# Optimization experiments

Hardware: AMD Instinct MI355X
Metric: run time of the kernel (lower is better)

The kernel has to match this reference:

```python
import jax, jax.numpy as jnp
import numpy as np

D = 1024       # num_feature == heads*dim_head
NHEADS = 16
HD = 64
INNER = NHEADS * HD
FF = 2048      # hardcoded mlp_dim in CSGO_model
L = 4          # depth
NOUT = 26      # hardcoded number of InvDynamic heads
IDH = 512      # inverse_dynamic_dim
B = 64
T = 32         # horizon


def _ln(x, g=None, b=None, eps=1e-5):
    mu = jnp.mean(x, axis=-1, keepdims=True)
    var = jnp.mean((x - mu) ** 2, axis=-1, keepdims=True)
    y = (x - mu) * jax.lax.rsqrt(var + eps)
    if g is not None:
        y = y * g + b
    return y


def setup_inputs() -> dict:
    key = jax.random.key(0)
    ks = jax.random.split(key, 20)
    s = 0.02
    inp = {
        'x': jax.random.normal(ks[0], (B, T, D), jnp.float32),
        # transformer params, stacked over depth L
        'qkv_w': jax.random.normal(ks[1], (L, D, 3 * INNER), jnp.float32) * s,
        'out_w': jax.random.normal(ks[2], (L, INNER, D), jnp.float32) * s,
        'out_b': jnp.zeros((L, D), jnp.float32),
        'attn_ln_g': jnp.ones((L, D), jnp.float32),
        'attn_ln_b': jnp.zeros((L, D), jnp.float32),
        'ff_ln_g': jnp.ones((L, D), jnp.float32),
        'ff_ln_b': jnp.zeros((L, D), jnp.float32),
        'ff_w1': jax.random.normal(ks[3], (L, D, FF), jnp.float32) * s,
        'ff_b1': jnp.zeros((L, FF), jnp.float32),
        'ff_w2': jax.random.normal(ks[4], (L, FF, D), jnp.float32) * s,
        'ff_b2': jnp.zeros((L, D), jnp.float32),
        # 26 InvDynamic heads, stacked
        'head_w1': jax.random.normal(ks[5], (NOUT, 2 * D, IDH), jnp.float32) * s,
        'head_b1': jnp.zeros((NOUT, IDH), jnp.float32),
        'head_w2': jax.random.normal(ks[6], (NOUT, IDH, IDH), jnp.float32) * s,
        'head_b2': jnp.zeros((NOUT, IDH), jnp.float32),
        'head_w3': jax.random.normal(ks[7], (NOUT, IDH, 1), jnp.float32) * s,
        'head_b3': jnp.zeros((NOUT, 1), jnp.float32),
    }
    return inp


def _forward(x, qkv_w, out_w, out_b, attn_ln_g, attn_ln_b, ff_ln_g, ff_ln_b,
             ff_w1, ff_b1, ff_w2, ff_b2,
             head_w1, head_b1, head_w2, head_b2, head_w3, head_b3):
    scale = HD ** -0.5

    def block(h, p):
        (qw, ow, ob, ag, ab, fg, fb, w1, b1, w2, b2) = p
        # x = attn(prenorm_ln(mid_ln(x))) + x  (mid LayerNorm has no affine, eps=1e-6)
        y = _ln(h, eps=1e-6)
        y = _ln(y, ag, ab)
        qkv = y @ qw                               # [B,T,3*INNER]
        q, k, v = jnp.split(qkv, 3, axis=-1)
        def split_heads(t):
            return t.reshape(t.shape[0], t.shape[1], NHEADS, HD).transpose(0, 2, 1, 3)
        q, k, v = split_heads(q), split_heads(k), split_heads(v)
        attn = jax.nn.softmax(jnp.einsum('bhqd,bhkd->bhqk', q, k) * scale, axis=-1)
        o = jnp.einsum('bhqk,bhkd->bhqd', attn, v)
        o = o.transpose(0, 2, 1, 3).reshape(h.shape[0], h.shape[1], INNER)
        h = h + (o @ ow + ob)
        # x = ff(prenorm_ln(x)) + x
        y = _ln(h, fg, fb)
        y = jax.nn.gelu(y @ w1 + b1, approximate=False) @ w2 + b2
        return h + y, None

    params = (qkv_w, out_w, out_b, attn_ln_g, attn_ln_b, ff_ln_g, ff_ln_b,
              ff_w1, ff_b1, ff_w2, ff_b2)
    x, _ = jax.lax.scan(block, x, params)

    # x_comb = concat(x[:,0], x[:,1])  -> [B, 2D]
    x_comb = jnp.concatenate([x[:, 0, :], x[:, 1, :]], axis=1)
    # 26 independent 3-layer MLP heads, batched as grouped GEMMs
    h1 = jax.nn.relu(jnp.einsum('bd,ndk->bnk', x_comb, head_w1) + head_b1)
    h2 = jax.nn.relu(jnp.einsum('bnk,nkj->bnj', h1, head_w2) + head_b2)
    out = jnp.einsum('bnk,nkj->bnj', h2, head_w3) + head_b3   # [B,26,1]
    return out


def reference(x, qkv_w, out_w, out_b, attn_ln_g, attn_ln_b, ff_ln_g, ff_ln_b,
              ff_w1, ff_b1, ff_w2, ff_b2,
              head_w1, head_b1, head_w2, head_b2, head_w3, head_b3):
    return _forward(x, qkv_w, out_w, out_b, attn_ln_g, attn_ln_b, ff_ln_g,
                    ff_ln_b, ff_w1, ff_b1, ff_w2, ff_b2,
                    head_w1, head_b1, head_w2, head_b2, head_w3, head_b3)
```

## Files before the change

kernel.cpp:

```cpp
#include <hip/hip_runtime.h>
#include <math.h>

static constexpr int BATCH = 64;
static constexpr int SEQ   = 32;
static constexpr int TOK   = BATCH * SEQ;
static constexpr int DIM   = 1024;
static constexpr int NH    = 16;
static constexpr int HDIM  = 64;
static constexpr int FFD   = 2048;
static constexpr int LAYERS= 4;
static constexpr int NHEAD_OUT = 26;
static constexpr int IDH   = 512;

typedef __bf16 bf16_t;
typedef __bf16 bf16x4 __attribute__((ext_vector_type(4)));
typedef __bf16 bf16x8 __attribute__((ext_vector_type(8)));
typedef float  f32x4  __attribute__((ext_vector_type(4)));
typedef float  f32x16 __attribute__((ext_vector_type(16)));
typedef unsigned short us4 __attribute__((ext_vector_type(4)));
typedef unsigned short us8 __attribute__((ext_vector_type(8)));

__device__ __forceinline__ unsigned short f2bfu(float f) {
    return __builtin_bit_cast(unsigned short, (bf16_t)f);
}

__device__ __forceinline__ void gload_lds16(const void* gp, void* lp) {
    __builtin_amdgcn_global_load_lds(
        (const __attribute__((address_space(1))) unsigned int*)gp,
        (__attribute__((address_space(3))) unsigned int*)lp,
        16, 0, 0);
}

__device__ __forceinline__ void tx_chunks4(const float* __restrict__ src,
                                           bf16_t* __restrict__ dst,
                                           int K, int N, int base4) {
    int nkb = K >> 6;
    int kk = threadIdx.x >> 6;
    int l  = threadIdx.x & 63;
    int nl = l & 31, k8 = (l >> 5) * 8;
    int base = base4 * 4;
    #pragma unroll
    for (int q = 0; q < 4; ++q) {
        int chunk = base + q;
        int ns = chunk / nkb;
        int kt = chunk - ns * nkb;
        int n = ns * 32 + nl;
        int kb = kt * 64 + kk * 16 + k8;
        us8 o;
        #pragma unroll
        for (int j = 0; j < 8; ++j)
            o[j] = f2bfu(src[(long)(kb + j) * N + n]);
        *(us8*)(dst + (long)chunk * 2048 + kk * 512 + l * 8) = o;
    }
}

struct TxPack {
    const float* src[4];
    bf16_t*      dst[4];
    int K[4], N[4];
    int blk0[4];
};

__global__ __launch_bounds__(256) void txd(TxPack p) {
    int bid = blockIdx.x;
    int s = 0;
    #pragma unroll
    for (int i = 1; i < 4; ++i) if (bid >= p.blk0[i]) s = i;
    tx_chunks4(p.src[s], p.dst[s], p.K[s], p.N[s], bid - p.blk0[s]);
}

__device__ __forceinline__ float block_sum(float v, float* red) {
    #pragma unroll
    for (int off = 32; off > 0; off >>= 1) v += __shfl_down(v, off);
    int lane = threadIdx.x & 63;
    int w    = threadIdx.x >> 6;
    if (lane == 0) red[w] = v;
    __syncthreads();
    float t = red[0] + red[1] + red[2] + red[3];
    __syncthreads();
    return t;
}

template<bool PRE, bool F32IN>
__global__ __launch_bounds__(256) void ln_kernel(const void* __restrict__ xv,
                                                 const float* __restrict__ g,
                                                 const float* __restrict__ b,
                                                 bf16_t* __restrict__ y,
                                                 bf16_t* __restrict__ hout) {
    __shared__ float red[4];
    long row = blockIdx.x;
    int tid = threadIdx.x;
    float4 v;
    if (F32IN) {
        const float* xr = (const float*)xv + row * DIM;
        v = *(const float4*)(xr + tid * 4);
        us4 hc;
        hc.x = f2bfu(v.x); hc.y = f2bfu(v.y); hc.z = f2bfu(v.z); hc.w = f2bfu(v.w);
        *(us4*)(hout + row * DIM + tid * 4) = hc;
        v.x = (float)(bf16_t)v.x; v.y = (float)(bf16_t)v.y;
        v.z = (float)(bf16_t)v.z; v.w = (float)(bf16_t)v.w;
    } else {
        const bf16_t* xr = (const bf16_t*)xv + row * DIM;
        bf16x4 r4 = *(const bf16x4*)(xr + tid * 4);
        v.x = (float)r4[0]; v.y = (float)r4[1]; v.z = (float)r4[2]; v.w = (float)r4[3];
    }
    if (PRE) {
        float s  = block_sum(v.x + v.y + v.z + v.w, red);
        float mu = s * (1.0f / DIM);
        v.x -= mu; v.y -= mu; v.z -= mu; v.w -= mu;
        float ss = block_sum(v.x*v.x + v.y*v.y + v.z*v.z + v.w*v.w, red);
        float r  = 1.0f / sqrtf(ss * (1.0f / DIM) + 1e-6f);
        v.x *= r; v.y *= r; v.z *= r; v.w *= r;
    }
    float s  = block_sum(v.x + v.y + v.z + v.w, red);
    float mu = s * (1.0f / DIM);
    v.x -= mu; v.y -= mu; v.z -= mu; v.w -= mu;
    float ss = block_sum(v.x*v.x + v.y*v.y + v.z*v.z + v.w*v.w, red);
    float r  = 1.0f / sqrtf(ss * (1.0f / DIM) + 1e-5f);
    float4 gg = *(const float4*)(g + tid * 4);
    float4 bb = *(const float4*)(b + tid * 4);
    us4 o;
    o.x = f2bfu(v.x * r * gg.x + bb.x);
    o.y = f2bfu(v.y * r * gg.y + bb.y);
    o.z = f2bfu(v.z * r * gg.z + bb.z);
    o.w = f2bfu(v.w * r * gg.w + bb.w);
    *(us4*)(y + row * DIM + tid * 4) = o;
}

template<int BM, int BN, int WM, int WN, int EPI>
__global__ __launch_bounds__(256) void gemm32(
    const bf16_t* __restrict__ A, const bf16_t* __restrict__ BT,
    const float* __restrict__ bias, const bf16_t* __restrict__ resid,
    bf16_t* __restrict__ Ch,
    int N, int K, int gemmBlocks, int gx,
    const float* __restrict__ txsrc, bf16_t* __restrict__ txdst,
    int txK, int txN)
{
    constexpr int WAVES_N = BN / WN;
    constexpr int FM = WM / 32, FN = WN / 32;
    constexpr int NSTG = BM / 32 + BN / 32;

    __shared__ bf16_t As[2][BM * 64];
    __shared__ bf16_t Bs[2][BN * 64];

    int bid = blockIdx.x;
    if (bid >= gemmBlocks) {
        tx_chunks4(txsrc, txdst, txK, txN, bid - gemmBlocks);
        return;
    }
    int bx = bid % gx, by = bid / gx;

    int tid  = threadIdx.x;
    int wave = tid >> 6, lane = tid & 63;
    int wr = wave / WAVES_N, wc = wave % WAVES_N;
    int m0 = by * BM, n0 = bx * BN;

    f32x16 acc[FM][FN];
    #pragma unroll
    for (int m = 0; m < FM; ++m)
        #pragma unroll
        for (int n = 0; n < FN; ++n)
            #pragma unroll
            for (int r = 0; r < 16; ++r)
                acc[m][n][r] = 0.f;

    long rsb = (long)K * 2;
    int  lr  = lane & 31;
    int  lkb = (lane >> 5) * 16;
    int  nkb = K >> 6;

    const char* Abase = (const char*)A + (long)(m0 + lr) * rsb + lkb;
    const char* Bbase = (const char*)BT + (long)(n0 >> 5) * nkb * 4096 + lane * 16;

    auto stage = [&](int c, int t) {
        long kb = (long)t * 128;
        #pragma unroll
        for (int i = 0; i < BM / 32; ++i) {
            int b = i * 4 + wave;
            gload_lds16(Abase + (long)(b >> 2) * 32 * rsb + (b & 3) * 32 + kb,
                        (char*)&As[c][0] + b * 1024);
        }
        #pragma unroll
        for (int i = 0; i < BN / 32; ++i) {
            int b = i * 4 + wave;
            gload_lds16(Bbase + ((long)(b >> 2) * nkb + t) * 4096 + (b & 3) * 1024,
                        (char*)&Bs[c][0] + b * 1024);
        }
    };

    int nt = K >> 6;
    stage(0, 0);
    int cur = 0;
    for (int t = 0; t < nt; ++t) {
        if (t + 1 < nt) {
            stage(cur ^ 1, t + 1);
            asm volatile("s_waitcnt vmcnt(%c0)" :: "i"(NSTG) : "memory");
        } else {
            asm volatile("s_waitcnt vmcnt(0)" ::: "memory");
        }
        __builtin_amdgcn_s_barrier();
        asm volatile("" ::: "memory");
        bf16x8 af[FM][4], bq[FN][4];
        #pragma unroll
        for (int m = 0; m < FM; ++m)
            #pragma unroll
            for (int kk = 0; kk < 4; ++kk)
                af[m][kk] = *(const bf16x8*)((const char*)&As[cur][0] +
                            ((wr * FM + m) * 4 + kk) * 1024 + (lane << 4));
        #pragma unroll
        for (int n = 0; n < FN; ++n)
            #pragma unroll
            for (int kk = 0; kk < 4; ++kk)
                bq[n][kk] = *(const bf16x8*)((const char*)&Bs[cur][0] +
                            ((wc * FN + n) * 4 + kk) * 1024 + (lane << 4));
        #pragma unroll
        for (int kk = 0; kk < 4; ++kk)
            #pragma unroll
            for (int m = 0; m < FM; ++m)
                #pragma unroll
                for (int n = 0; n < FN; ++n)
                    acc[m][n] = __builtin_amdgcn_mfma_f32_32x32x16_bf16(
                        af[m][kk], bq[n][kk], acc[m][n], 0, 0, 0);
        asm volatile("" ::: "memory");
        __builtin_amdgcn_s_barrier();
        cur ^= 1;
    }

    int rbase = 4 * (lane >> 5);
    #pragma unroll
    for (int m = 0; m < FM; ++m) {
        #pragma unroll
        for (int n = 0; n < FN; ++n) {
            int colI = n0 + wc * WN + n * 32 + (lane & 31);
            float bb = (EPI != 0) ? bias[colI] : 0.f;
            #pragma unroll
            for (int r = 0; r < 16; ++r) {
                int rowI = m0 + wr * WM + m * 32 + rbase + (r & 3) + 8 * (r >> 2);
                float v = acc[m][n][r] + bb;
                if (EPI == 2) v = 0.5f * v * (1.0f + erff(v * 0.70710678118654752f));
                long off = (long)rowI * N + colI;
                if (EPI == 1) v += (float)resid[off];
                Ch[off] = (bf16_t)v;
            }
        }
    }
}

__global__ __launch_bounds__(256) void gemm_hd(
    const bf16_t* __restrict__ A, const float* __restrict__ Bw,
    const float* __restrict__ bias, bf16_t* __restrict__ C,
    int N, int K, long aStride, long sA, long sB, long sbias, long sC)
{
    long g = blockIdx.z;
    A += g * sA;
    const float* Bp = Bw + g * sB;
    bias += g * sbias;
    bf16_t* Cp = C + g * sC;

    __shared__ bf16_t As[2][64 * 64];
    __shared__ float  Bf[2][64 * 64];

    int tid = threadIdx.x, wave = tid >> 6, lane = tid & 63;
    int wr = wave >> 1, wc = wave & 1;
    int n0 = blockIdx.x * 64;

    f32x4 acc[2][2];
    #pragma unroll
    for (int m = 0; m < 2; ++m)
        #pragma unroll
        for (int n = 0; n < 2; ++n)
            acc[m][n] = f32x4{0.f, 0.f, 0.f, 0.f};

    long rsb = aStride * 2;
    int  lr  = lane & 15;
    int  lkb = (lane >> 4) * 16;
    const char* Abase = (const char*)A + (long)lr * rsb + lkb;

    auto stage = [&](int c, int t) {
        long kb = (long)t * 128;
        #pragma unroll
        for (int i = 0; i < 2; ++i) {
            int b = i * 4 + wave;
            gload_lds16(Abase + (long)(b >> 1) * 16 * rsb + (b & 1) * 64 + kb,
                        (char*)&As[c][0] + b * 1024);
        }
        #pragma unroll
        for (int i = 0; i < 4; ++i) {
            int ch = i * 4 + wave;
            int row = ch * 4 + (lane >> 4);
            gload_lds16((const char*)Bp + ((long)(t * 64 + row) * N + n0) * 4 + (lane & 15) * 16,
                        (char*)&Bf[c][0] + ch * 1024);
        }
    };

    int nt = K >> 6;
    stage(0, 0);
    int cur = 0;
    for (int t = 0; t < nt; ++t) {
        if (t + 1 < nt) {
            stage(cur ^ 1, t + 1);
            asm volatile("s_waitcnt vmcnt(6)" ::: "memory");
        } else {
            asm volatile("s_waitcnt vmcnt(0)" ::: "memory");
        }
        __builtin_amdgcn_s_barrier();
        asm volatile("" ::: "memory");
        bf16x8 af[2][2], bq[2][2];
        #pragma unroll
        for (int m = 0; m < 2; ++m)
            #pragma unroll
            for (int h = 0; h < 2; ++h)
                af[m][h] = *(const bf16x8*)((const char*)&As[cur][0] +
                           ((wr * 2 + m) * 2 + h) * 1024 + (lane << 4));
        #pragma unroll
        for (int n = 0; n < 2; ++n) {
            int nl = wc * 32 + n * 16 + lr;
            #pragma unroll
            for (int h = 0; h < 2; ++h) {
                #pragma unroll
                for (int j = 0; j < 8; ++j) {
                    float v = Bf[cur][(h * 32 + (lane >> 4) * 8 + j) * 64 + nl];
                    bq[n][h][j] = (bf16_t)v;
                }
            }
        }
        #pragma unroll
        for (int h = 0; h < 2; ++h)
            #pragma unroll
            for (int m = 0; m < 2; ++m)
                #pragma unroll
                for (int n = 0; n < 2; ++n)
                    acc[m][n] = __builtin_amdgcn_mfma_f32_16x16x32_bf16(
                        af[m][h], bq[n][h], acc[m][n], 0, 0, 0);
        asm volatile("" ::: "memory");
        __builtin_amdgcn_s_barrier();
        cur ^= 1;
    }

    int lq = (lane >> 4) * 4;
    #pragma unroll
    for (int m = 0; m < 2; ++m) {
        #pragma unroll
        for (int n = 0; n < 2; ++n) {
            int colI = n0 + wc * 32 + n * 16 + lr;
            float bb = bias[colI];
            #pragma unroll
            for (int j = 0; j < 4; ++j) {
                int rowI = wr * 32 + m * 16 + lq + j;
                float v = fmaxf(acc[m][n][j] + bb, 0.0f);
                Cp[(long)rowI * N + colI] = (bf16_t)v;
            }
        }
    }
}

__global__ __launch_bounds__(256) void attn_kernel(const bf16_t* __restrict__ qkv,
                                                   bf16_t* __restrict__ o) {
    int bh = blockIdx.x;
    int b  = bh >> 4;
    int hh = bh & 15;
    __shared__ float qs[32][65];
    __shared__ float kt[64][36];
    __shared__ float vs[32][68];
    __shared__ float ps[32][33];
    const bf16_t* base = qkv + (long)b * SEQ * (3 * DIM) + hh * HDIM;
    int tid = threadIdx.x;

    {
        int t = tid >> 3, c = (tid & 7) * 8;
        bf16x8 qv = *(const bf16x8*)(base + (long)t * 3 * DIM + c);
        bf16x8 kv = *(const bf16x8*)(base + (long)t * 3 * DIM + DIM + c);
        bf16x8 vv = *(const bf16x8*)(base + (long)t * 3 * DIM + 2 * DIM + c);
        #pragma unroll
        for (int j = 0; j < 8; ++j) {
            int d = c + j;
            qs[t][d] = (float)qv[j];
            kt[d][(((t >> 2) ^ ((d >> 2) & 7)) << 2) + (t & 3)] = (float)kv[j];
            vs[t][d] = (float)vv[j];
        }
    }
    __syncthreads();

    {
        int r  = tid >> 3;
        int c0 = (tid & 7) * 4;
        f32x4 acc = {0.f, 0.f, 0.f, 0.f};
        #pragma unroll
        for (int d = 0; d < 64; ++d) {
            float qv = qs[r][d];
            float4 kv = *(const float4*)&kt[d][(((c0 >> 2) ^ ((d >> 2) & 7)) << 2)];
            acc[0] = fmaf(qv, kv.x, acc[0]);
            acc[1] = fmaf(qv, kv.y, acc[1]);
            acc[2] = fmaf(qv, kv.z, acc[2]);
            acc[3] = fmaf(qv, kv.w, acc[3]);
        }
        #pragma unroll
        for (int i = 0; i < 4; ++i) ps[r][c0 + i] = acc[i] * 0.125f;
    }
    __syncthreads();

    if (tid < 32) {
        float mx = -1e30f;
        for (int c = 0; c < 32; ++c) mx = fmaxf(mx, ps[tid][c]);
        float sum = 0.f;
        for (int c = 0; c < 32; ++c) { float e = expf(ps[tid][c] - mx); ps[tid][c] = e; sum += e; }
        float inv = 1.f / sum;
        for (int c = 0; c < 32; ++c) ps[tid][c] *= inv;
    }
    __syncthreads();

    {
        int r  = tid >> 3;
        int d0 = (tid & 7) * 8;
        float acc[8] = {};
        #pragma unroll
        for (int c = 0; c < 32; ++c) {
            float pv = ps[r][c];
            float4 v0 = *(const float4*)&vs[c][d0];
            float4 v1 = *(const float4*)&vs[c][d0 + 4];
            acc[0] = fmaf(pv, v0.x, acc[0]);
            acc[1] = fmaf(pv, v0.y, acc[1]);
            acc[2] = fmaf(pv, v0.z, acc[2]);
            acc[3] = fmaf(pv, v0.w, acc[3]);
            acc[4] = fmaf(pv, v1.x, acc[4]);
            acc[5] = fmaf(pv, v1.y, acc[5]);
            acc[6] = fmaf(pv, v1.z, acc[6]);
            acc[7] = fmaf(pv, v1.w, acc[7]);
        }
        us8 ov;
        #pragma unroll
        for (int j = 0; j < 8; ++j) ov[j] = f2bfu(acc[j]);
        *(us8*)(o + (long)b * SEQ * DIM + (long)r * DIM + hh * HDIM + d0) = ov;
    }
}

__global__ __launch_bounds__(256) void head3_kernel(const bf16_t* __restrict__ h2,
                                                    const float* __restrict__ w3,
                                                    const float* __restrict__ b3,
                                                    float* __restrict__ out) {
    int gid  = blockIdx.x * 256 + threadIdx.x;
    int wave = gid >> 6;
    int lane = gid & 63;
    if (wave >= NHEAD_OUT * BATCH) return;
    int n = wave >> 6;
    int b = wave & 63;
    const bf16_t* a = h2 + ((long)n * BATCH + b) * IDH;
    const float*  w = w3 + (long)n * IDH;
    float acc = 0.f;
    #pragma unroll
    for (int i = lane; i < IDH; i += 64) acc = fmaf((float)a[i], w[i], acc);
    #pragma unroll
    for (int off = 32; off > 0; off >>= 1) acc += __shfl_down(acc, off);
    if (lane == 0) out[b * NHEAD_OUT + n] = acc + b3[n];
}

extern "C" void kernel_launch(void* const* d_in, const int* in_sizes, int n_in,
                              void* d_out, int out_size, void* d_ws, size_t ws_size,
                              hipStream_t stream) {
    const float* x      = (const float*)d_in[0];
    const float* qkv_w  = (const float*)d_in[1];
    const float* out_w  = (const float*)d_in[2];
    const float* out_b  = (const float*)d_in[3];
    const float* attn_g = (const float*)d_in[4];
    const float* attn_b = (const float*)d_in[5];
    const float* ff_g   = (const float*)d_in[6];
    const float* ff_b   = (const float*)d_in[7];
    const float* ff_w1  = (const float*)d_in[8];
    const float* ff_b1  = (const float*)d_in[9];
    const float* ff_w2  = (const float*)d_in[10];
    const float* ff_b2  = (const float*)d_in[11];
    const float* hw1    = (const float*)d_in[12];
    const float* hb1    = (const float*)d_in[13];
    const float* hw2    = (const float*)d_in[14];
    const float* hb2    = (const float*)d_in[15];
    const float* hw3    = (const float*)d_in[16];
    const float* hb3    = (const float*)d_in[17];
    float* out = (float*)d_out;

    char* p = (char*)d_ws;
    bf16_t* h     = (bf16_t*)p;           p += (long)TOK * DIM * 2;
    bf16_t* qkvb  = (bf16_t*)p;           p += (long)TOK * 3 * DIM * 2;
    bf16_t* y     = (bf16_t*)p;           p += (long)TOK * DIM * 2;
    bf16_t* ob    = (bf16_t*)p;           p += (long)TOK * DIM * 2;
    bf16_t* ffb   = (bf16_t*)p;           p += (long)TOK * FFD * 2;
    bf16_t* h1    = (bf16_t*)p;           p += (long)NHEAD_OUT * BATCH * IDH * 2;
    bf16_t* h2    = (bf16_t*)p;           p += (long)NHEAD_OUT * BATCH * IDH * 2;
    bf16_t* qkvwt = (bf16_t*)p;           p += (long)LAYERS * DIM * 3 * DIM * 2;
    bf16_t* outwt = (bf16_t*)p;           p += (long)LAYERS * DIM * DIM * 2;
    bf16_t* ff1t  = (bf16_t*)p;           p += (long)LAYERS * DIM * FFD * 2;
    bf16_t* ff2t  = (bf16_t*)p;           p += (long)LAYERS * FFD * DIM * 2;

    const long sQ = (long)DIM * 3 * DIM;
    const long sO = (long)DIM * DIM;
    const long sF1 = (long)DIM * FFD;
    const long sF2 = (long)FFD * DIM;
    const int tbQ  = (3 * DIM / 32) * (DIM / 64) / 4;
    const int tbO  = (DIM / 32) * (DIM / 64) / 4;
    const int tbF1 = (FFD / 32) * (DIM / 64) / 4;
    const int tbF2 = (DIM / 32) * (FFD / 64) / 4;

    TxPack tp;
    tp.src[0] = qkv_w; tp.dst[0] = qkvwt; tp.K[0] = DIM; tp.N[0] = 3 * DIM;
    tp.src[1] = out_w; tp.dst[1] = outwt; tp.K[1] = DIM; tp.N[1] = DIM;
    tp.src[2] = ff_w1; tp.dst[2] = ff1t;  tp.K[2] = DIM; tp.N[2] = FFD;
    tp.src[3] = ff_w2; tp.dst[3] = ff2t;  tp.K[3] = FFD; tp.N[3] = DIM;
    tp.blk0[0] = 0;
    tp.blk0[1] = tbQ;
    tp.blk0[2] = tbQ + tbO;
    tp.blk0[3] = tbQ + tbO + tbF1;
    txd<<<tbQ + tbO + tbF1 + tbF2, 256, 0, stream>>>(tp);

    for (int l = 0; l < LAYERS; ++l) {
        bool more = (l + 1 < LAYERS);
        if (l == 0)
            ln_kernel<true, true><<<TOK, 256, 0, stream>>>(
                x, attn_g, attn_b, y, h);
        else
            ln_kernel<true, false><<<TOK, 256, 0, stream>>>(
                h, attn_g + l * DIM, attn_b + l * DIM, y, nullptr);

        {
            int gx = 3 * DIM / 128, gb = gx * (TOK / 64);
            gemm32<64, 128, 32, 64, 0><<<gb + (more ? tbQ : 0), 256, 0, stream>>>(
                y, qkvwt + l * sQ, nullptr, nullptr, qkvb,
                3 * DIM, DIM, gb, gx,
                qkv_w + (l + 1) * sQ, qkvwt + (l + 1) * sQ, DIM, 3 * DIM);
        }
        attn_kernel<<<BATCH * NH, 256, 0, stream>>>(qkvb, ob);
        {
            int gx = DIM / 64, gb = gx * (TOK / 64);
            gemm32<64, 64, 32, 32, 1><<<gb + (more ? tbO : 0), 256, 0, stream>>>(
                ob, outwt + l * sO, out_b + l * DIM, h, h,
                DIM, DIM, gb, gx,
                out_w + (l + 1) * sO, outwt + (l + 1) * sO, DIM, DIM);
        }
        ln_kernel<false, false><<<TOK, 256, 0, stream>>>(
            h, ff_g + l * DIM, ff_b + l * DIM, y, nullptr);
        {
            int gx = FFD / 128, gb = gx * (TOK / 64);
            gemm32<64, 128, 32, 64, 2><<<gb + (more ? tbF1 : 0), 256, 0, stream>>>(
                y, ff1t + l * sF1, ff_b1 + l * FFD, nullptr, ffb,
                FFD, DIM, gb, gx,
                ff_w1 + (l + 1) * sF1, ff1t + (l + 1) * sF1, DIM, FFD);
        }
        {
            int gx = DIM / 64, gb = gx * (TOK / 64);
            gemm32<64, 64, 32, 32, 1><<<gb + (more ? tbF2 : 0), 256, 0, stream>>>(
                ffb, ff2t + l * sF2, ff_b2 + l * DIM, h, h,
                DIM, FFD, gb, gx,
                ff_w2 + (l + 1) * sF2, ff2t + (l + 1) * sF2, FFD, DIM);
        }
    }

    gemm_hd<<<dim3(IDH / 64, 1, NHEAD_OUT), 256, 0, stream>>>(
        h, hw1, hb1, h1,
        IDH, 2 * DIM, (long)SEQ * DIM,
        0, (long)2 * DIM * IDH, IDH, (long)BATCH * IDH);
    gemm_hd<<<dim3(IDH / 64, 1, NHEAD_OUT), 256, 0, stream>>>(
        h1, hw2, hb2, h2,
        IDH, IDH, IDH,
        (long)BATCH * IDH, (long)IDH * IDH, IDH, (long)BATCH * IDH);
    head3_kernel<<<(NHEAD_OUT * BATCH * 64) / 256, 256, 0, stream>>>(h2, hw3, hb3, out);
}
```

Baseline: 518.6 us.

## Fold LayerNorm into GEMM epilogues via folded weights and per-row stats

Replaces the LayerNorm kernels that wrote a normalized bf16 activation with a lighter stats kernel (one wave per row) that stores only mean and inverse std. The LN gamma is folded into the transposed weights, and gamma·W and beta·W column sums are accumulated with atomics during weight conversion. The QKV and FF1 GEMMs then read the raw residual h and apply the normalization algebraically in the epilogue. This removes a full activation write and read per LN, at the cost of atomics in the transpose path and some numerical change from running the GEMM on the un-normalized bf16 input.

```diff
diff --git a/kernel.cpp b/kernel.cpp
--- a/kernel.cpp
+++ b/kernel.cpp
@@ -33,7 +33,11 @@
 
 __device__ __forceinline__ void tx_chunks4(const float* __restrict__ src,
                                            bf16_t* __restrict__ dst,
-                                           int K, int N, int base4) {
+                                           int K, int N, int base4,
+                                           const float* __restrict__ g,
+                                           const float* __restrict__ b,
+                                           float* __restrict__ c1,
+                                           float* __restrict__ c2) {
     int nkb = K >> 6;
     int kk = threadIdx.x >> 6;
     int l  = threadIdx.x & 63;
@@ -47,9 +51,24 @@
         int n = ns * 32 + nl;
         int kb = kt * 64 + kk * 16 + k8;
         us8 o;
-        #pragma unroll
-        for (int j = 0; j < 8; ++j)
-            o[j] = f2bfu(src[(long)(kb + j) * N + n]);
+        if (g != nullptr) {
+            float s1 = 0.f, s2 = 0.f;
+            #pragma unroll
+            for (int j = 0; j < 8; ++j) {
+                float w = src[(long)(kb + j) * N + n];
+                float gg = g[kb + j];
+                float sw = gg * w;
+                s1 += sw;
+                s2 += b[kb + j] * w;
+                o[j] = f2bfu(sw);
+            }
+            atomicAdd(&c1[n], s1);
+            atomicAdd(&c2[n], s2);
+        } else {
+            #pragma unroll
+            for (int j = 0; j < 8; ++j)
+                o[j] = f2bfu(src[(long)(kb + j) * N + n]);
+        }
         *(us8*)(dst + (long)chunk * 2048 + kk * 512 + l * 8) = o;
     }
 }
@@ -57,6 +76,10 @@
 struct TxPack {
     const float* src[4];
     bf16_t*      dst[4];
+    const float* g[4];
+    const float* b[4];
+    float*       c1[4];
+    float*       c2[4];
     int K[4], N[4];
     int blk0[4];
 };
@@ -66,75 +89,80 @@
     int s = 0;
     #pragma unroll
     for (int i = 1; i < 4; ++i) if (bid >= p.blk0[i]) s = i;
-    tx_chunks4(p.src[s], p.dst[s], p.K[s], p.N[s], bid - p.blk0[s]);
-}
-
-__device__ __forceinline__ float block_sum(float v, float* red) {
-    #pragma unroll
-    for (int off = 32; off > 0; off >>= 1) v += __shfl_down(v, off);
+    tx_chunks4(p.src[s], p.dst[s], p.K[s], p.N[s], bid - p.blk0[s],
+               p.g[s], p.b[s], p.c1[s], p.c2[s]);
+}
+
+template<bool DBL, bool F32IN>
+__global__ __launch_bounds__(256) void stats_kernel(const void* __restrict__ xv,
+                                                    bf16_t* __restrict__ hout,
+                                                    float2* __restrict__ st) {
+    int row  = blockIdx.x * 4 + (threadIdx.x >> 6);
     int lane = threadIdx.x & 63;
-    int w    = threadIdx.x >> 6;
-    if (lane == 0) red[w] = v;
-    __syncthreads();
-    float t = red[0] + red[1] + red[2] + red[3];
-    __syncthreads();
-    return t;
-}
-
-template<bool PRE, bool F32IN>
-__global__ __launch_bounds__(256) void ln_kernel(const void* __restrict__ xv,
-                                                 const float* __restrict__ g,
-                                                 const float* __restrict__ b,
-                                                 bf16_t* __restrict__ y,
-                                                 bf16_t* __restrict__ hout) {
-    __shared__ float red[4];
-    long row = blockIdx.x;
-    int tid = threadIdx.x;
-    float4 v;
+    float vals[16];
     if (F32IN) {
-        const float* xr = (const float*)xv + row * DIM;
-        v = *(const float4*)(xr + tid * 4);
-        us4 hc;
-        hc.x = f2bfu(v.x); hc.y = f2bfu(v.y); hc.z = f2bfu(v.z); hc.w = f2bfu(v.w);
-        *(us4*)(hout + row * DIM + tid * 4) = hc;
-        v.x = (float)(bf16_t)v.x; v.y = (float)(bf16_t)v.y;
-        v.z = (float)(bf16_t)v.z; v.w = (float)(bf16_t)v.w;
+        const float* xr = (const float*)xv + (long)row * DIM + lane * 16;
+        float4 a0 = *(const float4*)(xr);
+        float4 a1 = *(const float4*)(xr + 4);
+        float4 a2 = *(const float4*)(xr + 8);
+        float4 a3 = *(const float4*)(xr + 12);
+        float raw[16] = {a0.x,a0.y,a0.z,a0.w, a1.x,a1.y,a1.z,a1.w,
+                         a2.x,a2.y,a2.z,a2.w, a3.x,a3.y,a3.z,a3.w};
+        us8 o0, o1;
+        #pragma unroll
+        for (int j = 0; j < 8; ++j) { o0[j] = f2bfu(raw[j]); o1[j] = f2bfu(raw[8+j]); }
+        *(us8*)(hout + (long)row * DIM + lane * 16)     = o0;
+        *(us8*)(hout + (long)row * DIM + lane * 16 + 8) = o1;
+        #pragma unroll
+        for (int j = 0; j < 8; ++j) {
+            vals[j]     = (float)__builtin_bit_cast(bf16_t, o0[j]);
+            vals[8 + j] = (float)__builtin_bit_cast(bf16_t, o1[j]);
+        }
     } else {
-        const bf16_t* xr = (const bf16_t*)xv + row * DIM;
-        bf16x4 r4 = *(const bf16x4*)(xr + tid * 4);
-        v.x = (float)r4[0]; v.y = (float)r4[1]; v.z = (float)r4[2]; v.w = (float)r4[3];
-    }
-    if (PRE) {
-        float s  = block_sum(v.x + v.y + v.z + v.w, red);
-        float mu = s * (1.0f / DIM);
-        v.x -= mu; v.y -= mu; v.z -= mu; v.w -= mu;
-        float ss = block_sum(v.x*v.x + v.y*v.y + v.z*v.z + v.w*v.w, red);
-        float r  = 1.0f / sqrtf(ss * (1.0f / DIM) + 1e-6f);
-        v.x *= r; v.y *= r; v.z *= r; v.w *= r;
-    }
-    float s  = block_sum(v.x + v.y + v.z + v.w, red);
+        const bf16_t* xr = (const bf16_t*)xv + (long)row * DIM + lane * 16;
+        bf16x8 a = *(const bf16x8*)xr;
+        bf16x8 c = *(const bf16x8*)(xr + 8);
+        #pragma unroll
+        for (int j = 0; j < 8; ++j) { vals[j] = (float)a[j]; vals[8 + j] = (float)c[j]; }
+    }
+    float s = 0.f;
+    #pragma unroll
+    for (int j = 0; j < 16; ++j) s += vals[j];
+    #pragma unroll
+    for (int off = 32; off > 0; off >>= 1) s += __shfl_xor(s, off);
     float mu = s * (1.0f / DIM);
-    v.x -= mu; v.y -= mu; v.z -= mu; v.w -= mu;
-    float ss = block_sum(v.x*v.x + v.y*v.y + v.z*v.z + v.w*v.w, red);
-    float r  = 1.0f / sqrtf(ss * (1.0f / DIM) + 1e-5f);
-    float4 gg = *(const float4*)(g + tid * 4);
-    float4 bb = *(const float4*)(b + tid * 4);
-    us4 o;
-    o.x = f2bfu(v.x * r * gg.x + bb.x);
-    o.y = f2bfu(v.y * r * gg.y + bb.y);
-    o.z = f2bfu(v.z * r * gg.z + bb.z);
-    o.w = f2bfu(v.w * r * gg.w + bb.w);
-    *(us4*)(y + row * DIM + tid * 4) = o;
-}
+    float ss = 0.f;
+    #pragma unroll
+    for (int j = 0; j < 16; ++j) { float d = vals[j] - mu; ss += d * d; }
+    #pragma unroll
+    for (int off = 32; off > 0; off >>= 1) ss += __shfl_xor(ss, off);
+    if (lane == 0) {
+        float var = ss * (1.0f / DIM);
+        float R;
+        if (DBL) {
+            float inv1 = 1.0f / sqrtf(var + 1e-6f);
+            float var2 = var * inv1 * inv1;
+            R = inv1 * (1.0f / sqrtf(var2 + 1e-5f));
+        } else {
+            R = 1.0f / sqrtf(var + 1e-5f);
+        }
+        st[row] = float2{mu, R};
+    }
+}
+
 
 template<int BM, int BN, int WM, int WN, int EPI>
 __global__ __launch_bounds__(256) void gemm32(
     const bf16_t* __restrict__ A, const bf16_t* __restrict__ BT,
     const float* __restrict__ bias, const bf16_t* __restrict__ resid,
     bf16_t* __restrict__ Ch,
+    const float2* __restrict__ stats,
+    const float* __restrict__ c1, const float* __restrict__ c2,
     int N, int K, int gemmBlocks, int gx,
     const float* __restrict__ txsrc, bf16_t* __restrict__ txdst,
-    int txK, int txN)
+    int txK, int txN,
+    const float* __restrict__ txg, const float* __restrict__ txb,
+    float* __restrict__ txc1, float* __restrict__ txc2)
 {
     constexpr int WAVES_N = BN / WN;
     constexpr int FM = WM / 32, FN = WN / 32;
@@ -145,7 +173,7 @@
 
     int bid = blockIdx.x;
     if (bid >= gemmBlocks) {
-        tx_chunks4(txsrc, txdst, txK, txN, bid - gemmBlocks);
+        tx_chunks4(txsrc, txdst, txK, txN, bid - gemmBlocks, txg, txb, txc1, txc2);
         return;
     }
     int bx = bid % gx, by = bid / gx;
@@ -232,14 +260,22 @@
         #pragma unroll
         for (int n = 0; n < FN; ++n) {
             int colI = n0 + wc * WN + n * 32 + (lane & 31);
-            float bb = (EPI != 0) ? bias[colI] : 0.f;
+            float cc1 = 0.f, cc2 = 0.f, bb = 0.f;
+            if (EPI == 0 || EPI == 2) { cc1 = c1[colI]; cc2 = c2[colI]; }
+            if (EPI == 1 || EPI == 2) bb = bias[colI];
             #pragma unroll
             for (int r = 0; r < 16; ++r) {
                 int rowI = m0 + wr * WM + m * 32 + rbase + (r & 3) + 8 * (r >> 2);
-                float v = acc[m][n][r] + bb;
-                if (EPI == 2) v = 0.5f * v * (1.0f + erff(v * 0.70710678118654752f));
+                float v = acc[m][n][r];
                 long off = (long)rowI * N + colI;
-                if (EPI == 1) v += (float)resid[off];
+                if (EPI == 1) {
+                    v += bb + (float)resid[off];
+                } else {
+                    float2 stv = stats[rowI];
+                    v = stv.y * v - stv.y * stv.x * cc1 + cc2 + bb;
+                    if (EPI == 2)
+                        v = 0.5f * v * (1.0f + erff(v * 0.70710678118654752f));
+                }
                 Ch[off] = (bf16_t)v;
             }
         }
@@ -480,7 +516,6 @@
     char* p = (char*)d_ws;
     bf16_t* h     = (bf16_t*)p;           p += (long)TOK * DIM * 2;
     bf16_t* qkvb  = (bf16_t*)p;           p += (long)TOK * 3 * DIM * 2;
-    bf16_t* y     = (bf16_t*)p;           p += (long)TOK * DIM * 2;
     bf16_t* ob    = (bf16_t*)p;           p += (long)TOK * DIM * 2;
     bf16_t* ffb   = (bf16_t*)p;           p += (long)TOK * FFD * 2;
     bf16_t* h1    = (bf16_t*)p;           p += (long)NHEAD_OUT * BATCH * IDH * 2;
@@ -489,6 +524,14 @@
     bf16_t* outwt = (bf16_t*)p;           p += (long)LAYERS * DIM * DIM * 2;
     bf16_t* ff1t  = (bf16_t*)p;           p += (long)LAYERS * DIM * FFD * 2;
     bf16_t* ff2t  = (bf16_t*)p;           p += (long)LAYERS * FFD * DIM * 2;
+    float2* stQ   = (float2*)p;           p += (long)TOK * 8;
+    float2* stF   = (float2*)p;           p += (long)TOK * 8;
+    float*  cbuf  = (float*)p;
+    float*  c1q   = cbuf;
+    float*  c2q   = c1q + (long)LAYERS * 3 * DIM;
+    float*  c1f   = c2q + (long)LAYERS * 3 * DIM;
+    float*  c2f   = c1f + (long)LAYERS * FFD;
+    size_t  cbytes = ((long)LAYERS * (3 * DIM + 3 * DIM + FFD + FFD)) * 4;
 
     const long sQ = (long)DIM * 3 * DIM;
     const long sO = (long)DIM * DIM;
@@ -499,11 +542,17 @@
     const int tbF1 = (FFD / 32) * (DIM / 64) / 4;
     const int tbF2 = (DIM / 32) * (FFD / 64) / 4;
 
+    hipMemsetAsync(cbuf, 0, cbytes, stream);
+
     TxPack tp;
     tp.src[0] = qkv_w; tp.dst[0] = qkvwt; tp.K[0] = DIM; tp.N[0] = 3 * DIM;
+    tp.g[0] = attn_g; tp.b[0] = attn_b; tp.c1[0] = c1q; tp.c2[0] = c2q;
     tp.src[1] = out_w; tp.dst[1] = outwt; tp.K[1] = DIM; tp.N[1] = DIM;
+    tp.g[1] = nullptr; tp.b[1] = nullptr; tp.c1[1] = nullptr; tp.c2[1] = nullptr;
     tp.src[2] = ff_w1; tp.dst[2] = ff1t;  tp.K[2] = DIM; tp.N[2] = FFD;
+    tp.g[2] = ff_g; tp.b[2] = ff_b; tp.c1[2] = c1f; tp.c2[2] = c2f;
     tp.src[3] = ff_w2; tp.dst[3] = ff2t;  tp.K[3] = FFD; tp.N[3] = DIM;
+    tp.g[3] = nullptr; tp.b[3] = nullptr; tp.c1[3] = nullptr; tp.c2[3] = nullptr;
     tp.blk0[0] = 0;
     tp.blk0[1] = tbQ;
     tp.blk0[2] = tbQ + tbO;
@@ -512,43 +561,52 @@
 
     for (int l = 0; l < LAYERS; ++l) {
         bool more = (l + 1 < LAYERS);
+        int ln = more ? (l + 1) : l;
+
         if (l == 0)
-            ln_kernel<true, true><<<TOK, 256, 0, stream>>>(
-                x, attn_g, attn_b, y, h);
+            stats_kernel<true, true><<<TOK / 4, 256, 0, stream>>>(x, h, stQ);
         else
-            ln_kernel<true, false><<<TOK, 256, 0, stream>>>(
-                h, attn_g + l * DIM, attn_b + l * DIM, y, nullptr);
+            stats_kernel<true, false><<<TOK / 4, 256, 0, stream>>>(h, nullptr, stQ);
 
         {
             int gx = 3 * DIM / 128, gb = gx * (TOK / 64);
             gemm32<64, 128, 32, 64, 0><<<gb + (more ? tbQ : 0), 256, 0, stream>>>(
-                y, qkvwt + l * sQ, nullptr, nullptr, qkvb,
+                h, qkvwt + l * sQ, nullptr, nullptr, qkvb,
+                stQ, c1q + l * 3 * DIM, c2q + l * 3 * DIM,
                 3 * DIM, DIM, gb, gx,
-                qkv_w + (l + 1) * sQ, qkvwt + (l + 1) * sQ, DIM, 3 * DIM);
+                qkv_w + ln * sQ, qkvwt + ln * sQ, DIM, 3 * DIM,
+                attn_g + ln * DIM, attn_b + ln * DIM,
+                c1q + ln * 3 * DIM, c2q + ln * 3 * DIM);
         }
         attn_kernel<<<BATCH * NH, 256, 0, stream>>>(qkvb, ob);
         {
             int gx = DIM / 64, gb = gx * (TOK / 64);
             gemm32<64, 64, 32, 32, 1><<<gb + (more ? tbO : 0), 256, 0, stream>>>(
                 ob, outwt + l * sO, out_b + l * DIM, h, h,
+                nullptr, nullptr, nullptr,
                 DIM, DIM, gb, gx,
-                out_w + (l + 1) * sO, outwt + (l + 1) * sO, DIM, DIM);
-        }
-        ln_kernel<false, false><<<TOK, 256, 0, stream>>>(
-            h, ff_g + l * DIM, ff_b + l * DIM, y, nullptr);
+                out_w + ln * sO, outwt + ln * sO, DIM, DIM,
+                nullptr, nullptr, nullptr, nullptr);
+        }
+        stats_kernel<false, false><<<TOK / 4, 256, 0, stream>>>(h, nullptr, stF);
         {
             int gx = FFD / 128, gb = gx * (TOK / 64);
             gemm32<64, 128, 32, 64, 2><<<gb + (more ? tbF1 : 0), 256, 0, stream>>>(
-                y, ff1t + l * sF1, ff_b1 + l * FFD, nullptr, ffb,
+                h, ff1t + l * sF1, ff_b1 + l * FFD, nullptr, ffb,
+                stF, c1f + l * FFD, c2f + l * FFD,
                 FFD, DIM, gb, gx,
-                ff_w1 + (l + 1) * sF1, ff1t + (l + 1) * sF1, DIM, FFD);
+                ff_w1 + ln * sF1, ff1t + ln * sF1, DIM, FFD,
+                ff_g + ln * DIM, ff_b + ln * DIM,
+                c1f + ln * FFD, c2f + ln * FFD);
         }
         {
             int gx = DIM / 64, gb = gx * (TOK / 64);
             gemm32<64, 64, 32, 32, 1><<<gb + (more ? tbF2 : 0), 256, 0, stream>>>(
                 ffb, ff2t + l * sF2, ff_b2 + l * DIM, h, h,
+                nullptr, nullptr, nullptr,
                 DIM, FFD, gb, gx,
-                ff_w2 + (l + 1) * sF2, ff2t + (l + 1) * sF2, FFD, DIM);
+                ff_w2 + ln * sF2, ff2t + ln * sF2, FFD, DIM,
+                nullptr, nullptr, nullptr, nullptr);
         }
     }
 
```

Result: slower. 603.2 us (+16.3%).

## Shift weight-transpose work one GEMM earlier to overlap with compute

Applied to the files above, without the earlier changes.

Replaces the upfront transpose of all four first-layer weight matrices with a single transpose of only the QKV weights. Each GEMM launch now carries extra blocks that convert the weights needed by the next GEMM in the same layer (out_w, ff_w1, ff_w2), and the last GEMM of each layer converts the next layer's QKV weights. This shrinks the serial prologue and spreads conversion work across the pipeline. The risk is that tighter dependencies leave less slack, since the next kernel's weights must be ready as soon as the current kernel finishes.

```diff
diff --git a/kernel.cpp b/kernel.cpp
--- a/kernel.cpp
+++ b/kernel.cpp
@@ -54,19 +54,10 @@
     }
 }
 
-struct TxPack {
-    const float* src[4];
-    bf16_t*      dst[4];
-    int K[4], N[4];
-    int blk0[4];
-};
-
-__global__ __launch_bounds__(256) void txd(TxPack p) {
-    int bid = blockIdx.x;
-    int s = 0;
-    #pragma unroll
-    for (int i = 1; i < 4; ++i) if (bid >= p.blk0[i]) s = i;
-    tx_chunks4(p.src[s], p.dst[s], p.K[s], p.N[s], bid - p.blk0[s]);
+__global__ __launch_bounds__(256) void txd1(const float* __restrict__ src,
+                                            bf16_t* __restrict__ dst,
+                                            int K, int N) {
+    tx_chunks4(src, dst, K, N, blockIdx.x);
 }
 
 __device__ __forceinline__ float block_sum(float v, float* red) {
@@ -499,16 +490,7 @@
     const int tbF1 = (FFD / 32) * (DIM / 64) / 4;
     const int tbF2 = (DIM / 32) * (FFD / 64) / 4;
 
-    TxPack tp;
-    tp.src[0] = qkv_w; tp.dst[0] = qkvwt; tp.K[0] = DIM; tp.N[0] = 3 * DIM;
-    tp.src[1] = out_w; tp.dst[1] = outwt; tp.K[1] = DIM; tp.N[1] = DIM;
-    tp.src[2] = ff_w1; tp.dst[2] = ff1t;  tp.K[2] = DIM; tp.N[2] = FFD;
-    tp.src[3] = ff_w2; tp.dst[3] = ff2t;  tp.K[3] = FFD; tp.N[3] = DIM;
-    tp.blk0[0] = 0;
-    tp.blk0[1] = tbQ;
-    tp.blk0[2] = tbQ + tbO;
-    tp.blk0[3] = tbQ + tbO + tbF1;
-    txd<<<tbQ + tbO + tbF1 + tbF2, 256, 0, stream>>>(tp);
+    txd1<<<tbQ, 256, 0, stream>>>(qkv_w, qkvwt, DIM, 3 * DIM);
 
     for (int l = 0; l < LAYERS; ++l) {
         bool more = (l + 1 < LAYERS);
@@ -521,34 +503,34 @@
 
         {
             int gx = 3 * DIM / 128, gb = gx * (TOK / 64);
-            gemm32<64, 128, 32, 64, 0><<<gb + (more ? tbQ : 0), 256, 0, stream>>>(
+            gemm32<64, 128, 32, 64, 0><<<gb + tbO, 256, 0, stream>>>(
                 y, qkvwt + l * sQ, nullptr, nullptr, qkvb,
                 3 * DIM, DIM, gb, gx,
-                qkv_w + (l + 1) * sQ, qkvwt + (l + 1) * sQ, DIM, 3 * DIM);
+                out_w + l * sO, outwt + l * sO, DIM, DIM);
         }
         attn_kernel<<<BATCH * NH, 256, 0, stream>>>(qkvb, ob);
         {
             int gx = DIM / 64, gb = gx * (TOK / 64);
-            gemm32<64, 64, 32, 32, 1><<<gb + (more ? tbO : 0), 256, 0, stream>>>(
+            gemm32<64, 64, 32, 32, 1><<<gb + tbF1, 256, 0, stream>>>(
                 ob, outwt + l * sO, out_b + l * DIM, h, h,
                 DIM, DIM, gb, gx,
-                out_w + (l + 1) * sO, outwt + (l + 1) * sO, DIM, DIM);
+                ff_w1 + l * sF1, ff1t + l * sF1, DIM, FFD);
         }
         ln_kernel<false, false><<<TOK, 256, 0, stream>>>(
             h, ff_g + l * DIM, ff_b + l * DIM, y, nullptr);
         {
             int gx = FFD / 128, gb = gx * (TOK / 64);
-            gemm32<64, 128, 32, 64, 2><<<gb + (more ? tbF1 : 0), 256, 0, stream>>>(
+            gemm32<64, 128, 32, 64, 2><<<gb + tbF2, 256, 0, stream>>>(
                 y, ff1t + l * sF1, ff_b1 + l * FFD, nullptr, ffb,
                 FFD, DIM, gb, gx,
-                ff_w1 + (l + 1) * sF1, ff1t + (l + 1) * sF1, DIM, FFD);
+                ff_w2 + l * sF2, ff2t + l * sF2, FFD, DIM);
         }
         {
             int gx = DIM / 64, gb = gx * (TOK / 64);
-            gemm32<64, 64, 32, 32, 1><<<gb + (more ? tbF2 : 0), 256, 0, stream>>>(
+            gemm32<64, 64, 32, 32, 1><<<gb + (more ? tbQ : 0), 256, 0, stream>>>(
                 ffb, ff2t + l * sF2, ff_b2 + l * DIM, h, h,
                 DIM, FFD, gb, gx,
-                ff_w2 + (l + 1) * sF2, ff2t + (l + 1) * sF2, FFD, DIM);
+                qkv_w + (l + 1) * sQ, qkvwt + (l + 1) * sQ, DIM, 3 * DIM);
         }
     }
 
```

After: 515.0 us (median of 2 runs). No clear change (-0.7%).
